# Kernel tuning notes

Measured on AMD Instinct MI355X. Metric: run time of the kernel, lower is better.

Reference implementation:

```python
import jax, jax.numpy as jnp
import numpy as np


def setup_inputs() -> dict:
    key = jax.random.key(0)
    ks = jax.random.split(key, 7)
    b, c, t, h, w = 2, 64, 8, 32, 32
    d = 64
    return {
        "video_features": jax.random.normal(ks[0], (b, c, t, h, w), dtype=jnp.float32),
        "wq": jax.random.normal(ks[1], (d, c), dtype=jnp.float32) * 0.05,
        "bq": jax.random.normal(ks[2], (d,), dtype=jnp.float32) * 0.05,
        "wk": jax.random.normal(ks[3], (d, c), dtype=jnp.float32) * 0.05,
        "bk": jax.random.normal(ks[4], (d,), dtype=jnp.float32) * 0.05,
        "wv": jax.random.normal(ks[5], (d, c), dtype=jnp.float32) * 0.05,
        "bv": jax.random.normal(ks[6], (d,), dtype=jnp.float32) * 0.05,
    }


def reference(video_features, wq, bq, wk, bk, wv, bv):
    b, c, t, h, w = video_features.shape
    d = wq.shape[0]
    xf = video_features.reshape(b, c, t * h * w)  # [b, c, N]
    # 1x1x1 Conv3d == channel-wise linear projection
    q = jnp.einsum('dc,bcn->bnd', wq, xf) + bq                 # [b, N, d]
    k = jnp.einsum('dc,bcn->bnd', wk, xf) + bk                 # [b, N, d]
    v = jnp.einsum('dc,bcn->bnd', wv, xf) + bv                 # [b, N, d]
    scores = jnp.einsum('bnd,bmd->bnm', q, k) / jnp.sqrt(jnp.asarray(d, xf.dtype))  # [b, N, N]
    attn = jax.nn.softmax(scores, axis=-1)
    out = jnp.einsum('bnm,bmd->bnd', attn, v)                  # [b, N, d]
    out = out.transpose(0, 2, 1).reshape(b, d, t, h, w)
    out = out.sum(axis=2).reshape(b, d, 1, h, w)
    return out
```

## Files before the change

### kernel.cpp

```cpp
#include <hip/hip_runtime.h>
#include <math.h>

#define B 2
#define D 64
#define N 8192
#define T 8
#define HW 1024
#define NCH 8
#define KPC (N / NCH)
#define KT 64
#define NT (KPC / KT)
#define QT 256
#define NQT (N / QT)

#define LOG2E 1.44269504f

typedef _Float16 half8 __attribute__((ext_vector_type(8)));
typedef _Float16 half4 __attribute__((ext_vector_type(4)));
typedef _Float16 half2 __attribute__((ext_vector_type(2)));
typedef float floatx4 __attribute__((ext_vector_type(4)));
typedef unsigned uint2v __attribute__((ext_vector_type(2)));

__global__ __launch_bounds__(256)
void proj_kernel(const float* __restrict__ x,
                 const float* __restrict__ wq, const float* __restrict__ bq,
                 const float* __restrict__ wk, const float* __restrict__ bk,
                 const float* __restrict__ wv, const float* __restrict__ bv,
                 _Float16* __restrict__ Qh, _Float16* __restrict__ Kh,
                 _Float16* __restrict__ VTh) {
    int n  = blockIdx.x * 256 + threadIdx.x;
    int d0 = blockIdx.y * 4;
    int b  = blockIdx.z;

    float xcol[64];
    const float* xb = x + (size_t)b * 64 * N + n;
#pragma unroll
    for (int c = 0; c < 64; ++c) xcol[c] = xb[(size_t)c * N];

    float aq[4], ak[4], av[4];
#pragma unroll
    for (int i = 0; i < 4; ++i) { aq[i] = bq[d0+i]; ak[i] = bk[d0+i]; av[i] = bv[d0+i]; }
#pragma unroll
    for (int c = 0; c < 64; ++c) {
        float xv = xcol[c];
#pragma unroll
        for (int i = 0; i < 4; ++i) {
            aq[i] += wq[(d0 + i) * 64 + c] * xv;
            ak[i] += wk[(d0 + i) * 64 + c] * xv;
            av[i] += wv[(d0 + i) * 64 + c] * xv;
        }
    }
    size_t rowb = ((size_t)b * N + n) * 64 + d0;
    half4 hq, hk;
    const float qs = 0.125f * LOG2E;
#pragma unroll
    for (int i = 0; i < 4; ++i) {
        hq[i] = (_Float16)(aq[i] * qs);
        hk[i] = (_Float16)ak[i];
    }
    *(half4*)(Qh + rowb) = hq;
    *(half4*)(Kh + rowb) = hk;
#pragma unroll
    for (int i = 0; i < 4; ++i)
        VTh[((size_t)b * 64 + d0 + i) * N + n] = (_Float16)av[i];
}

__global__ __launch_bounds__(256, 2)
void attn_kernel(const _Float16* __restrict__ Qh, const _Float16* __restrict__ Kh,
                 const _Float16* __restrict__ VTh,
                 _Float16* __restrict__ Opart, float* __restrict__ lpart) {
    __shared__ _Float16 Ks[2][64][72];
    __shared__ _Float16 VTs[2][64][72];

    int bid = blockIdx.x;
    int b   = bid / (NCH * NQT);
    int rem = bid % (NCH * NQT);
    int ch  = rem / NQT;
    int qt  = rem % NQT;
    int q0  = qt * QT;
    int kbase = ch * KPC;

    int tid  = threadIdx.x;
    int wave = tid >> 6;
    int lane = tid & 63;
    int L    = lane & 15;
    int quad = lane >> 4;

    half8 qa[4][2];
#pragma unroll
    for (int g = 0; g < 4; ++g) {
        const _Float16* qrow = Qh + ((size_t)b * N + q0 + wave * 64 + g * 16 + L) * 64;
        qa[g][0] = *(const half8*)(qrow + quad * 8);
        qa[g][1] = *(const half8*)(qrow + 32 + quad * 8);
    }

    floatx4 o[4][4];
    floatx4 lacc[4];
#pragma unroll
    for (int g = 0; g < 4; ++g) {
        lacc[g] = (floatx4)0.f;
#pragma unroll
        for (int s = 0; s < 4; ++s) o[g][s] = (floatx4)0.f;
    }

    half8 ones;
    {
        _Float16 v = (L == 0) ? (_Float16)1.0f : (_Float16)0.0f;
#pragma unroll
        for (int i = 0; i < 8; ++i) ones[i] = v;
    }

    int srow = tid >> 2, sseg = tid & 3;
    const _Float16* Kg = Kh  + (size_t)b * N * 64 + (size_t)sseg * 16;
    const _Float16* Vg = VTh + ((size_t)b * 64 + srow) * N + sseg * 16;

    half8 kr0, kr1, vr0, vr1;
    {
        const _Float16* kp = Kg + (size_t)(kbase + srow) * 64;
        kr0 = *(const half8*)(kp);
        kr1 = *(const half8*)(kp + 8);
        const _Float16* vp = Vg + kbase;
        vr0 = *(const half8*)(vp);
        vr1 = *(const half8*)(vp + 8);
    }
    *(half8*)(&Ks[0][srow][sseg * 16])      = kr0;
    *(half8*)(&Ks[0][srow][sseg * 16 + 8])  = kr1;
    *(half8*)(&VTs[0][srow][sseg * 16])     = vr0;
    *(half8*)(&VTs[0][srow][sseg * 16 + 8]) = vr1;
    __syncthreads();

    for (int kt = 0; kt < NT; ++kt) {
        int cur = kt & 1, nxt = cur ^ 1;
        bool more = (kt + 1 < NT);

        if (more) {
            int kb = kbase + (kt + 1) * KT;
            const _Float16* kp = Kg + (size_t)(kb + srow) * 64;
            kr0 = *(const half8*)(kp);
            kr1 = *(const half8*)(kp + 8);
            const _Float16* vp = Vg + kb;
            vr0 = *(const half8*)(vp);
            vr1 = *(const half8*)(vp + 8);
        }

        half8 kf[4][2], vb[4][2];
#pragma unroll
        for (int sub = 0; sub < 4; ++sub) {
            kf[sub][0] = *(const half8*)(&Ks[cur][sub * 16 + L][quad * 8]);
            kf[sub][1] = *(const half8*)(&Ks[cur][sub * 16 + L][32 + quad * 8]);
            vb[sub][0] = *(const half8*)(&VTs[cur][sub * 16 + L][quad * 8]);
            vb[sub][1] = *(const half8*)(&VTs[cur][sub * 16 + L][32 + quad * 8]);
        }

#pragma unroll
        for (int p = 0; p < 2; ++p) {
            floatx4 s[2][4];
#pragma unroll
            for (int sub = 0; sub < 4; ++sub) {
#pragma unroll
                for (int gg = 0; gg < 2; ++gg) {
                    int g = 2 * p + gg;
                    floatx4 acc = (floatx4)0.f;
                    acc = __builtin_amdgcn_mfma_f32_16x16x32_f16(kf[sub][0], qa[g][0], acc, 0, 0, 0);
                    acc = __builtin_amdgcn_mfma_f32_16x16x32_f16(kf[sub][1], qa[g][1], acc, 0, 0, 0);
                    s[gg][sub] = acc;
                }
            }

#pragma unroll
            for (int gg = 0; gg < 2; ++gg)
#pragma unroll
                for (int sub = 0; sub < 4; ++sub)
#pragma unroll
                    for (int r = 0; r < 4; ++r)
                        s[gg][sub][r] = __builtin_amdgcn_exp2f(s[gg][sub][r]);

            half8 pa[2][2];
#pragma unroll
            for (int gg = 0; gg < 2; ++gg) {
                unsigned ph[4][2];
#pragma unroll
                for (int sub = 0; sub < 4; ++sub) {
                    auto p0 = __builtin_amdgcn_cvt_pkrtz(s[gg][sub][0], s[gg][sub][1]);
                    auto p1 = __builtin_amdgcn_cvt_pkrtz(s[gg][sub][2], s[gg][sub][3]);
                    ph[sub][0] = __builtin_bit_cast(unsigned, p0);
                    ph[sub][1] = __builtin_bit_cast(unsigned, p1);
                }
#if __has_builtin(__builtin_amdgcn_permlane32_swap) && __has_builtin(__builtin_amdgcn_permlane16_swap)
#pragma unroll
                for (int h = 0; h < 2; ++h) {
                    uint2v s0 = __builtin_amdgcn_permlane32_swap(ph[2 * h][0], ph[2 * h + 1][0], false, false);
                    uint2v r0 = __builtin_amdgcn_permlane16_swap(s0[0], s0[1], false, false);
                    uint2v s1 = __builtin_amdgcn_permlane32_swap(ph[2 * h][1], ph[2 * h + 1][1], false, false);
                    uint2v r1 = __builtin_amdgcn_permlane16_swap(s1[0], s1[1], false, false);
                    union { half8 v; unsigned w[4]; } u;
                    u.w[0] = r0[0];
                    u.w[1] = r1[0];
                    u.w[2] = r0[1];
                    u.w[3] = r1[1];
                    pa[gg][h] = u.v;
                }
#else
                {
                    _Float16* Pb = gg ? &VTs[nxt][wave * 16][0] : &Ks[nxt][wave * 16][0];
#pragma unroll
                    for (int sub = 0; sub < 4; ++sub) {
                        int cb = L * 72 + sub * 16 + quad * 4;
                        *(unsigned*)(&Pb[cb])     = ph[sub][0];
                        *(unsigned*)(&Pb[cb + 2]) = ph[sub][1];
                    }
#pragma unroll
                    for (int h = 0; h < 2; ++h)
                        pa[gg][h] = *(const half8*)(&Pb[L * 72 + h * 32 + quad * 8]);
                }
#endif
            }

#pragma unroll
            for (int sub = 0; sub < 4; ++sub) {
#pragma unroll
                for (int gg = 0; gg < 2; ++gg) {
                    int g = 2 * p + gg;
                    o[g][sub] = __builtin_amdgcn_mfma_f32_16x16x32_f16(pa[gg][0], vb[sub][0], o[g][sub], 0, 0, 0);
                    o[g][sub] = __builtin_amdgcn_mfma_f32_16x16x32_f16(pa[gg][1], vb[sub][1], o[g][sub], 0, 0, 0);
                }
            }
#pragma unroll
            for (int gg = 0; gg < 2; ++gg) {
                int g = 2 * p + gg;
                lacc[g] = __builtin_amdgcn_mfma_f32_16x16x32_f16(pa[gg][0], ones, lacc[g], 0, 0, 0);
                lacc[g] = __builtin_amdgcn_mfma_f32_16x16x32_f16(pa[gg][1], ones, lacc[g], 0, 0, 0);
            }
        }

        if (more) {
            *(half8*)(&Ks[nxt][srow][sseg * 16])      = kr0;
            *(half8*)(&Ks[nxt][srow][sseg * 16 + 8])  = kr1;
            *(half8*)(&VTs[nxt][srow][sseg * 16])     = vr0;
            *(half8*)(&VTs[nxt][srow][sseg * 16 + 8]) = vr1;
        }
        __syncthreads();
    }

    size_t pb = (size_t)(b * NCH + ch) * N + q0 + wave * 64;
#pragma unroll
    for (int g = 0; g < 4; ++g)
#pragma unroll
        for (int sub = 0; sub < 4; ++sub)
#pragma unroll
            for (int r = 0; r < 4; ++r)
                Opart[(pb + g * 16 + quad * 4 + r) * 64 + sub * 16 + L] =
                    (_Float16)o[g][sub][r];
    if (L == 0) {
#pragma unroll
        for (int g = 0; g < 4; ++g)
#pragma unroll
            for (int r = 0; r < 4; ++r)
                lpart[pb + g * 16 + quad * 4 + r] = lacc[g][r];
    }
}

__global__ void reduce_kernel(const _Float16* __restrict__ Opart,
                              const float* __restrict__ lpart,
                              float* __restrict__ out) {
    int g  = blockIdx.x * 256 + threadIdx.x;
    int dp = (g & 31) * 2;
    int hw = (g >> 5) & (HW - 1);
    int b  = g >> 15;

    float a0 = 0.f, a1 = 0.f;
    for (int t = 0; t < T; ++t) {
        int row = t * HW + hw;
        float Lsum = 0.f, n0 = 0.f, n1 = 0.f;
#pragma unroll
        for (int c = 0; c < NCH; ++c) {
            size_t pb = (size_t)(b * NCH + c) * N + row;
            Lsum += lpart[pb];
            half2 v = *(const half2*)(Opart + pb * 64 + dp);
            n0 += (float)v[0];
            n1 += (float)v[1];
        }
        a0 += n0 / Lsum;
        a1 += n1 / Lsum;
    }
    out[((size_t)b * D + dp) * HW + hw]     = a0;
    out[((size_t)b * D + dp + 1) * HW + hw] = a1;
}

extern "C" void kernel_launch(void* const* d_in, const int* in_sizes, int n_in,
                              void* d_out, int out_size, void* d_ws, size_t ws_size,
                              hipStream_t stream) {
    const float* x  = (const float*)d_in[0];
    const float* wq = (const float*)d_in[1];
    const float* bq = (const float*)d_in[2];
    const float* wk = (const float*)d_in[3];
    const float* bk = (const float*)d_in[4];
    const float* wv = (const float*)d_in[5];
    const float* bv = (const float*)d_in[6];

    const size_t QSZ = (size_t)B * N * 64;
    _Float16* Qh    = (_Float16*)d_ws;
    _Float16* Kh    = Qh + QSZ;
    _Float16* VTh   = Kh + QSZ;
    _Float16* Opart = VTh + QSZ;
    float*    lpart = (float*)(Opart + (size_t)B * NCH * N * 64);

    proj_kernel<<<dim3(N / 256, 16, B), 256, 0, stream>>>(x, wq, bq, wk, bk, wv, bv,
                                                          Qh, Kh, VTh);
    attn_kernel<<<B * NCH * NQT, 256, 0, stream>>>(Qh, Kh, VTh, Opart, lpart);
    reduce_kernel<<<(B * HW * D / 2) / 256, 256, 0, stream>>>(Opart, lpart, (float*)d_out);
}
```

Baseline: 125.9 us.

## Stage K/V tiles via global_load_lds with XOR-swizzled LDS layout

Replaces the register-staged K/V tile prefetch with direct global-to-LDS loads (global_load_lds, 16 bytes per lane) when the builtin is available. The padded [64][72] LDS layout becomes a dense 64x64 layout with an XOR swizzle on 16-byte chunks to avoid bank conflicts on the fragment reads. It also drops the LDS fallback for P transposition, so the permlane builtins are now required. The aim is to cut VGPR pressure and the separate ds_write instructions, at the cost of relying on correct wait/ordering for the async LDS writes before the barrier.

```diff
diff --git a/kernel.cpp b/kernel.cpp
--- a/kernel.cpp
+++ b/kernel.cpp
@@ -65,12 +65,22 @@
         VTh[((size_t)b * 64 + d0 + i) * N + n] = (_Float16)av[i];
 }
 
+#if __has_builtin(__builtin_amdgcn_global_load_lds)
+#define HAVE_GLL 1
+typedef const __attribute__((address_space(1))) void* gas1_t;
+typedef __attribute__((address_space(3))) void* las3_t;
+#define GLOAD16(g, l) \
+    __builtin_amdgcn_global_load_lds((gas1_t)(const void*)(g), (las3_t)(void*)(l), 16, 0, 0)
+#else
+#define HAVE_GLL 0
+#endif
+
 __global__ __launch_bounds__(256, 2)
 void attn_kernel(const _Float16* __restrict__ Qh, const _Float16* __restrict__ Kh,
                  const _Float16* __restrict__ VTh,
                  _Float16* __restrict__ Opart, float* __restrict__ lpart) {
-    __shared__ _Float16 Ks[2][64][72];
-    __shared__ _Float16 VTs[2][64][72];
+    __shared__ _Float16 Ks[2][4096];
+    __shared__ _Float16 VTs[2][4096];
 
     int bid = blockIdx.x;
     int b   = bid / (NCH * NQT);
@@ -85,6 +95,7 @@
     int lane = tid & 63;
     int L    = lane & 15;
     int quad = lane >> 4;
+    int swz  = L & 7;
 
     half8 qa[4][2];
 #pragma unroll
@@ -110,46 +121,52 @@
         for (int i = 0; i < 8; ++i) ones[i] = v;
     }
 
-    int srow = tid >> 2, sseg = tid & 3;
-    const _Float16* Kg = Kh  + (size_t)b * N * 64 + (size_t)sseg * 16;
-    const _Float16* Vg = VTh + ((size_t)b * 64 + srow) * N + sseg * 16;
-
-    half8 kr0, kr1, vr0, vr1;
-    {
-        const _Float16* kp = Kg + (size_t)(kbase + srow) * 64;
-        kr0 = *(const half8*)(kp);
-        kr1 = *(const half8*)(kp + 8);
-        const _Float16* vp = Vg + kbase;
-        vr0 = *(const half8*)(vp);
-        vr1 = *(const half8*)(vp + 8);
-    }
-    *(half8*)(&Ks[0][srow][sseg * 16])      = kr0;
-    *(half8*)(&Ks[0][srow][sseg * 16 + 8])  = kr1;
-    *(half8*)(&VTs[0][srow][sseg * 16])     = vr0;
-    *(half8*)(&VTs[0][srow][sseg * 16 + 8]) = vr1;
+    int s0 = (wave * 2 + 0) * 64 + lane;
+    int s1 = (wave * 2 + 1) * 64 + lane;
+    int r0 = s0 >> 3, c0 = (s0 & 7) ^ (r0 & 7);
+    int r1 = s1 >> 3, c1 = (s1 & 7) ^ (r1 & 7);
+    const _Float16* kSrc0 = Kh + (size_t)b * N * 64 + (size_t)r0 * 64 + c0 * 8;
+    const _Float16* kSrc1 = Kh + (size_t)b * N * 64 + (size_t)r1 * 64 + c1 * 8;
+    const _Float16* vSrc0 = VTh + ((size_t)b * 64 + r0) * N + c0 * 8;
+    const _Float16* vSrc1 = VTh + ((size_t)b * 64 + r1) * N + c1 * 8;
+
+#if HAVE_GLL
+#define STAGE_TILE(buf, kb) do { \
+        GLOAD16(kSrc0 + (size_t)(kb) * 64, &Ks[buf][(wave * 2 + 0) * 512]); \
+        GLOAD16(kSrc1 + (size_t)(kb) * 64, &Ks[buf][(wave * 2 + 1) * 512]); \
+        GLOAD16(vSrc0 + (kb),              &VTs[buf][(wave * 2 + 0) * 512]); \
+        GLOAD16(vSrc1 + (kb),              &VTs[buf][(wave * 2 + 1) * 512]); \
+    } while (0)
+#else
+#define STAGE_TILE(buf, kb) do { \
+        half8 k0 = *(const half8*)(kSrc0 + (size_t)(kb) * 64); \
+        half8 k1 = *(const half8*)(kSrc1 + (size_t)(kb) * 64); \
+        half8 v0 = *(const half8*)(vSrc0 + (kb)); \
+        half8 v1 = *(const half8*)(vSrc1 + (kb)); \
+        *(half8*)(&Ks[buf][s0 * 8])  = k0; \
+        *(half8*)(&Ks[buf][s1 * 8])  = k1; \
+        *(half8*)(&VTs[buf][s0 * 8]) = v0; \
+        *(half8*)(&VTs[buf][s1 * 8]) = v1; \
+    } while (0)
+#endif
+
+    STAGE_TILE(0, kbase);
     __syncthreads();
 
     for (int kt = 0; kt < NT; ++kt) {
         int cur = kt & 1, nxt = cur ^ 1;
         bool more = (kt + 1 < NT);
 
-        if (more) {
-            int kb = kbase + (kt + 1) * KT;
-            const _Float16* kp = Kg + (size_t)(kb + srow) * 64;
-            kr0 = *(const half8*)(kp);
-            kr1 = *(const half8*)(kp + 8);
-            const _Float16* vp = Vg + kb;
-            vr0 = *(const half8*)(vp);
-            vr1 = *(const half8*)(vp + 8);
-        }
+        if (more) STAGE_TILE(nxt, kbase + (kt + 1) * KT);
 
         half8 kf[4][2], vb[4][2];
 #pragma unroll
         for (int sub = 0; sub < 4; ++sub) {
-            kf[sub][0] = *(const half8*)(&Ks[cur][sub * 16 + L][quad * 8]);
-            kf[sub][1] = *(const half8*)(&Ks[cur][sub * 16 + L][32 + quad * 8]);
-            vb[sub][0] = *(const half8*)(&VTs[cur][sub * 16 + L][quad * 8]);
-            vb[sub][1] = *(const half8*)(&VTs[cur][sub * 16 + L][32 + quad * 8]);
+            int rb = (sub * 16 + L) * 64;
+            kf[sub][0] = *(const half8*)(&Ks[cur][rb + ((quad)     ^ swz) * 8]);
+            kf[sub][1] = *(const half8*)(&Ks[cur][rb + ((4 + quad) ^ swz) * 8]);
+            vb[sub][0] = *(const half8*)(&VTs[cur][rb + ((quad)     ^ swz) * 8]);
+            vb[sub][1] = *(const half8*)(&VTs[cur][rb + ((4 + quad) ^ swz) * 8]);
         }
 
 #pragma unroll
@@ -186,34 +203,19 @@
                     ph[sub][0] = __builtin_bit_cast(unsigned, p0);
                     ph[sub][1] = __builtin_bit_cast(unsigned, p1);
                 }
-#if __has_builtin(__builtin_amdgcn_permlane32_swap) && __has_builtin(__builtin_amdgcn_permlane16_swap)
 #pragma unroll
                 for (int h = 0; h < 2; ++h) {
-                    uint2v s0 = __builtin_amdgcn_permlane32_swap(ph[2 * h][0], ph[2 * h + 1][0], false, false);
-                    uint2v r0 = __builtin_amdgcn_permlane16_swap(s0[0], s0[1], false, false);
-                    uint2v s1 = __builtin_amdgcn_permlane32_swap(ph[2 * h][1], ph[2 * h + 1][1], false, false);
-                    uint2v r1 = __builtin_amdgcn_permlane16_swap(s1[0], s1[1], false, false);
+                    uint2v t0 = __builtin_amdgcn_permlane32_swap(ph[2 * h][0], ph[2 * h + 1][0], false, false);
+                    uint2v w0 = __builtin_amdgcn_permlane16_swap(t0[0], t0[1], false, false);
+                    uint2v t1 = __builtin_amdgcn_permlane32_swap(ph[2 * h][1], ph[2 * h + 1][1], false, false);
+                    uint2v w1 = __builtin_amdgcn_permlane16_swap(t1[0], t1[1], false, false);
                     union { half8 v; unsigned w[4]; } u;
-                    u.w[0] = r0[0];
-                    u.w[1] = r1[0];
-                    u.w[2] = r0[1];
-                    u.w[3] = r1[1];
+                    u.w[0] = w0[0];
+                    u.w[1] = w1[0];
+                    u.w[2] = w0[1];
+                    u.w[3] = w1[1];
                     pa[gg][h] = u.v;
                 }
-#else
-                {
-                    _Float16* Pb = gg ? &VTs[nxt][wave * 16][0] : &Ks[nxt][wave * 16][0];
-#pragma unroll
-                    for (int sub = 0; sub < 4; ++sub) {
-                        int cb = L * 72 + sub * 16 + quad * 4;
-                        *(unsigned*)(&Pb[cb])     = ph[sub][0];
-                        *(unsigned*)(&Pb[cb + 2]) = ph[sub][1];
-                    }
-#pragma unroll
-                    for (int h = 0; h < 2; ++h)
-                        pa[gg][h] = *(const half8*)(&Pb[L * 72 + h * 32 + quad * 8]);
-                }
-#endif
             }
 
 #pragma unroll
@@ -233,12 +235,6 @@
             }
         }
 
-        if (more) {
-            *(half8*)(&Ks[nxt][srow][sseg * 16])      = kr0;
-            *(half8*)(&Ks[nxt][srow][sseg * 16 + 8])  = kr1;
-            *(half8*)(&VTs[nxt][srow][sseg * 16])     = vr0;
-            *(half8*)(&VTs[nxt][srow][sseg * 16 + 8]) = vr1;
-        }
         __syncthreads();
     }
 
```

Result: slower. 128.9 us (+2.4%).
